# Optimization experiments

Measured on AMD Instinct MI355X. Metric: run time of the kernel, lower is better.

Reference implementation:

```python
import jax, jax.numpy as jnp
import numpy as np

N, E, D_IN, D_H, D_OUT = 100000, 1600000, 128, 128, 16


def setup_inputs() -> dict:
    key = jax.random.key(0)
    k_x, k_e, k_w1, k_w2 = jax.random.split(key, 4)
    x = jax.random.normal(k_x, (N, D_IN), dtype=jnp.float32)
    edge_index = jax.random.randint(k_e, (2, E), 0, N, dtype=jnp.int64)
    # glorot-ish init for the two GCNConv weight matrices
    W1 = jax.random.normal(k_w1, (D_IN, D_H), dtype=jnp.float32) * (1.0 / np.sqrt(D_IN))
    b1 = jnp.zeros((D_H,), dtype=jnp.float32)
    W2 = jax.random.normal(k_w2, (D_H, D_OUT), dtype=jnp.float32) * (1.0 / np.sqrt(D_H))
    b2 = jnp.zeros((D_OUT,), dtype=jnp.float32)
    return {"x": x, "edge_index": edge_index, "W1": W1, "b1": b1, "W2": W2, "b2": b2}


def _gcn_conv(x, src, dst, norm, W, b, n):
    # linear transform, gather from source nodes, normalize, scatter-add to targets
    h = x @ W                                   # [N, d_out]
    msg = h[src] * norm[:, None]                # [E+N, d_out]
    return jax.ops.segment_sum(msg, dst, num_segments=n) + b


def reference(x, edge_index, W1, b1, W2, b2):
    n = x.shape[0]
    # GCNConv default: add self-loops, symmetric normalization D^-1/2 A D^-1/2
    loops = jnp.arange(n, dtype=edge_index.dtype)
    src = jnp.concatenate([edge_index[0], loops])
    dst = jnp.concatenate([edge_index[1], loops])
    deg = jax.ops.segment_sum(jnp.ones_like(dst, dtype=x.dtype), dst, num_segments=n)
    dinv = jnp.where(deg > 0, jax.lax.rsqrt(deg), 0.0)
    norm = dinv[src] * dinv[dst]                # [E+N]

    h = _gcn_conv(x, src, dst, norm, W1, b1, n)
    h = jax.nn.relu(h)
    # dropout is identity in eval mode (reference uses eval / deterministic path)
    out = _gcn_conv(h, src, dst, norm, W2, b2, n)
    return out
```

## Files before the change

### kernel.cpp

```cpp
#include <hip/hip_runtime.h>

typedef unsigned int uint;
typedef __attribute__((ext_vector_type(8))) short bf16x8;
typedef __attribute__((ext_vector_type(4))) float f32x4;

#define D_IN 128
#define D_H  128
#define D_OUT 16
#define NPC 512
#define NPCSH 9
#define CLDS 224
#define P1 256
#define XL_STRIDE 68
#define WT_STRIDE 68

static __device__ __forceinline__ float bflo(uint u) { return __uint_as_float(u << 16); }
static __device__ __forceinline__ float bfhi(uint u) { return __uint_as_float(u & 0xFFFF0000u); }
static __device__ __forceinline__ uint f2bf(float f) {
    uint b = __float_as_uint(f);
    return (b + 0x7FFFu + ((b >> 16) & 1u)) >> 16;
}
static __device__ __forceinline__ uint pk(float a, float b) {
    return f2bf(a) | (f2bf(b) << 16);
}


__global__ __launch_bounds__(256) void k_p1hist(const int* __restrict__ dst, int E, int N, int C,
                                                int chunk, int* __restrict__ hist1,
                                                const float* __restrict__ W1,
                                                uint* __restrict__ W1p) {
    __shared__ int h[CLDS];
    int t = threadIdx.x, b = blockIdx.x;
    if (b >= P1) {
        int p = (b - P1) * 256 + t;
        int k2 = p >> 7, f = p & 127;
        float w0 = W1[(size_t)(2 * k2) * 128 + f];
        float w1 = W1[(size_t)(2 * k2 + 1) * 128 + f];
        W1p[p] = pk(w0, w1);
        return;
    }
    for (int i = t; i < C; i += 256) h[i] = 0;
    __syncthreads();
    int e0 = b * chunk, e1 = min(e0 + chunk, E);
    for (int e = e0 + t; e < e1; e += 256) {
        int d = dst[e];
        d = max(0, min(d, N - 1));
        atomicAdd(&h[d >> NPCSH], 1);
    }
    __syncthreads();
    for (int i = t; i < C; i += 256) hist1[(size_t)i * P1 + b] = h[i];
}

__global__ __launch_bounds__(1024) void k_p1scan(int* __restrict__ hist1, int C,
                                                 int* __restrict__ cbase) {
    __shared__ int col[CLDS];
    __shared__ int sdata[1024];
    int t = threadIdx.x;
    int w = t >> 6, lane = t & 63;
    for (int i = w; i < C; i += 16) {
        int4 v = ((const int4*)hist1)[i * 64 + lane];
        int s = v.x + v.y + v.z + v.w;
        int inc = s;
        for (int off = 1; off < 64; off <<= 1) {
            int o = __shfl_up(inc, off);
            if (lane >= off) inc += o;
        }
        int excl = inc - s;
        int4 p;
        p.x = excl;
        p.y = excl + v.x;
        p.z = excl + v.x + v.y;
        p.w = excl + v.x + v.y + v.z;
        ((int4*)hist1)[i * 64 + lane] = p;
        if (lane == 63) col[i] = inc;
    }
    __syncthreads();
    int v = (t < C) ? col[t] : 0;
    sdata[t] = v;
    __syncthreads();
    for (int off = 1; off < 1024; off <<= 1) {
        int x = (t >= off) ? sdata[t - off] : 0;
        __syncthreads();
        sdata[t] += x;
        __syncthreads();
    }
    int pos = sdata[t] - v;
    if (t < C) cbase[t] = pos;
    if (t == 1023) cbase[C] = sdata[1023];
    if (t < C) col[t] = pos;
    __syncthreads();
    for (int i = w; i < C; i += 16) {
        int base = col[i];
        int4 p = ((int4*)hist1)[i * 64 + lane];
        p.x += base; p.y += base; p.z += base; p.w += base;
        ((int4*)hist1)[i * 64 + lane] = p;
    }
}

__global__ __launch_bounds__(256) void k_p1fill(const int* __restrict__ src,
                                                const int* __restrict__ dst, int E, int N, int C,
                                                int chunk, const int* __restrict__ hist1,
                                                uint* __restrict__ binned1) {
    __shared__ int cur[CLDS];
    int t = threadIdx.x, b = blockIdx.x;
    for (int i = t; i < C; i += 256) cur[i] = hist1[(size_t)i * P1 + b];
    __syncthreads();
    int e0 = b * chunk, e1 = min(e0 + chunk, E);
    for (int e = e0 + t; e < e1; e += 256) {
        int d = dst[e];
        d = max(0, min(d, N - 1));
        int s = src[e];
        s = max(0, min(s, N - 1));
        int p = atomicAdd(&cur[d >> NPCSH], 1);
        binned1[p] = ((uint)(d & (NPC - 1)) << 17) | (uint)s;
    }
}


__global__ __launch_bounds__(256) void k_p2gemm1(const uint* __restrict__ binned1,
                                                 const int* __restrict__ cbase, int N, int C,
                                                 int* __restrict__ ssrc, int* __restrict__ rowptr,
                                                 int* __restrict__ deg, float* __restrict__ dinv,
                                                 const uint* __restrict__ W1p,
                                                 const float* __restrict__ x,
                                                 uint* __restrict__ hs_b, int ntiles) {
    __shared__ uint smem[128 * WT_STRIDE + 64 * XL_STRIDE];
    int t = threadIdx.x;
    if ((int)blockIdx.x < C) {
        int* ncnt = (int*)smem;
        int* nbase_ = ncnt + NPC;
        int* sdata = nbase_ + NPC;
        int c = blockIdx.x;
        int start = cbase[c], end = cbase[c + 1];
        for (int i = t; i < NPC; i += 256) ncnt[i] = 0;
        __syncthreads();
        for (int j = start + t; j < end; j += 256) atomicAdd(&ncnt[binned1[j] >> 17], 1);
        __syncthreads();
        int v0 = ncnt[2 * t], v1 = ncnt[2 * t + 1];
        int s = v0 + v1;
        sdata[t] = s;
        __syncthreads();
        for (int off = 1; off < 256; off <<= 1) {
            int xv = (t >= off) ? sdata[t - off] : 0;
            __syncthreads();
            sdata[t] += xv;
            __syncthreads();
        }
        int pre = sdata[t] - s;
        nbase_[2 * t] = start + pre;
        nbase_[2 * t + 1] = start + pre + v0;
        __syncthreads();
        for (int i = t; i < NPC; i += 256) {
            int node = c * NPC + i;
            if (node < N) {
                deg[node] = ncnt[i];
                rowptr[node] = nbase_[i];
                dinv[node] = rsqrtf((float)ncnt[i] + 1.0f);
            }
        }
        __syncthreads();
        for (int i = t; i < NPC; i += 256) ncnt[i] = nbase_[i];
        __syncthreads();
        for (int j = start + t; j < end; j += 256) {
            uint pe = binned1[j];
            int p = atomicAdd(&ncnt[pe >> 17], 1);
            ssrc[p] = (int)(pe & 0x1FFFFu);
        }
        return;
    }
    uint* Wt = smem;
    uint* xl = smem + 128 * WT_STRIDE;
    int role = blockIdx.x - C;
    int nroles = gridDim.x - C;
    for (int p = t; p < 64 * 128; p += 256) {
        int k2 = p >> 7, f = p & 127;
        Wt[f * WT_STRIDE + k2] = W1p[p];
    }
    int w = t >> 6, lane = t & 63;
    int q = lane >> 4, m = lane & 15;
    const float4* x4 = (const float4*)x;
    for (int tile = role; tile < ntiles; tile += nroles) {
        int row0 = tile * 64;
        __syncthreads();
        for (int p = t; p < 64 * 32; p += 256) {
            int r = p >> 5, c2 = p & 31;
            int gr = row0 + r;
            float4 v = (gr < N) ? x4[(size_t)gr * 32 + c2] : make_float4(0.f, 0.f, 0.f, 0.f);
            *(uint2*)&xl[r * XL_STRIDE + 2 * c2] = make_uint2(pk(v.x, v.y), pk(v.z, v.w));
        }
        __syncthreads();
        bf16x8 afr[4][4];
#pragma unroll
        for (int rt = 0; rt < 4; rt++)
#pragma unroll
            for (int kc = 0; kc < 4; kc++)
                afr[rt][kc] = *(const bf16x8*)&xl[(rt * 16 + m) * XL_STRIDE + kc * 16 + q * 4];
        f32x4 acc[2][4];
#pragma unroll
        for (int c = 0; c < 2; c++)
#pragma unroll
            for (int rt = 0; rt < 4; rt++) acc[c][rt] = (f32x4){0.f, 0.f, 0.f, 0.f};
#pragma unroll
        for (int c = 0; c < 2; c++) {
            int f = w * 32 + c * 16 + m;
#pragma unroll
            for (int kc = 0; kc < 4; kc++) {
                bf16x8 bfr = *(const bf16x8*)&Wt[f * WT_STRIDE + kc * 16 + q * 4];
#pragma unroll
                for (int rt = 0; rt < 4; rt++)
                    acc[c][rt] = __builtin_amdgcn_mfma_f32_16x16x32_bf16(afr[rt][kc], bfr,
                                                                         acc[c][rt], 0, 0, 0);
            }
        }
        __syncthreads();
        uint* outl = xl;
#pragma unroll
        for (int rt = 0; rt < 4; rt++) {
#pragma unroll
            for (int c = 0; c < 2; c++) {
                f32x4 a = acc[c][rt];
#pragma unroll
                for (int r = 0; r < 4; r++) {
                    float v = a[r];
                    float vn = __shfl_xor(v, 1);
                    if (!(lane & 1)) {
                        int row = rt * 16 + q * 4 + r;
                        int cp = (w * 32 + c * 16 + m) >> 1;
                        outl[row * 65 + cp] = pk(v, vn);
                    }
                }
            }
        }
        __syncthreads();
        for (int p = t; p < 64 * 64; p += 256) {
            int r = p >> 6, cc = p & 63;
            int gr = row0 + r;
            if (gr < N) hs_b[(size_t)gr * 64 + cc] = outl[r * 65 + cc];
        }
    }
}


__global__ __launch_bounds__(256) void k_agg1(const uint* __restrict__ hs_b,
                                              const int* __restrict__ rowptr,
                                              const int* __restrict__ deg,
                                              const int* __restrict__ ssrc,
                                              const float* __restrict__ dinv,
                                              const float2* __restrict__ b1, int N,
                                              uint* __restrict__ rh_b) {
    int w = threadIdx.x >> 6, lane = threadIdx.x & 63;
    int d = blockIdx.x * 4 + w;
    if (d >= N) return;
    int start = rowptr[d], cnt = deg[d];
    float sc = dinv[d];
    uint sv = hs_b[(size_t)d * 64 + lane];
    float a0 = bflo(sv) * sc, a1 = bfhi(sv) * sc;
    int base = 0;
    while (base < cnt) {
        int nb = min(cnt - base, 64);
        int idxv = (lane < nb) ? ssrc[start + base + lane] : 0;
        float dvv = dinv[idxv];
        int j = 0;
        for (; j + 16 <= nb; j += 16) {
            uint u[16];
            float dv[16];
#pragma unroll
            for (int q = 0; q < 16; q++) {
                int i = __shfl(idxv, j + q);
                dv[q] = __shfl(dvv, j + q);
                u[q] = hs_b[(size_t)i * 64 + lane];
            }
#pragma unroll
            for (int q = 0; q < 16; q++) {
                a0 = fmaf(bflo(u[q]), dv[q], a0);
                a1 = fmaf(bfhi(u[q]), dv[q], a1);
            }
        }
        for (; j + 4 <= nb; j += 4) {
            uint u[4];
            float dv[4];
#pragma unroll
            for (int q = 0; q < 4; q++) {
                int i = __shfl(idxv, j + q);
                dv[q] = __shfl(dvv, j + q);
                u[q] = hs_b[(size_t)i * 64 + lane];
            }
#pragma unroll
            for (int q = 0; q < 4; q++) {
                a0 = fmaf(bflo(u[q]), dv[q], a0);
                a1 = fmaf(bfhi(u[q]), dv[q], a1);
            }
        }
        for (; j < nb; j++) {
            int i = __shfl(idxv, j);
            float dv = __shfl(dvv, j);
            uint u = hs_b[(size_t)i * 64 + lane];
            a0 = fmaf(bflo(u), dv, a0);
            a1 = fmaf(bfhi(u), dv, a1);
        }
        base += nb;
    }
    float2 bb = b1[lane];
    rh_b[(size_t)d * 64 + lane] =
        pk(fmaxf(fmaf(a0, sc, bb.x), 0.f), fmaxf(fmaf(a1, sc, bb.y), 0.f));
}


__global__ __launch_bounds__(256) void k_gemm2(const uint* __restrict__ rh_b,
                                               const float* __restrict__ W2,
                                               const float* __restrict__ dinv, int N,
                                               uint* __restrict__ h2_b) {
    __shared__ float Wl[D_H * D_OUT];
    int t = threadIdx.x;
    for (int i = t; i < D_H * D_OUT; i += 256) Wl[i] = W2[i];
    __syncthreads();
    int r = blockIdx.x * 256 + t;
    if (r >= N) return;
    const uint* xrow = rh_b + (size_t)r * 64;
    float acc[16];
#pragma unroll
    for (int f = 0; f < 16; f++) acc[f] = 0.f;
    for (int c = 0; c < 16; c++) {
        uint4 xv = *(const uint4*)(xrow + c * 4);
        uint xs[4] = {xv.x, xv.y, xv.z, xv.w};
#pragma unroll
        for (int u = 0; u < 4; u++) {
            int k = c * 8 + u * 2;
            float x0 = bflo(xs[u]), x1 = bfhi(xs[u]);
            const float* w0 = &Wl[k * 16];
            const float* w1 = &Wl[(k + 1) * 16];
#pragma unroll
            for (int f = 0; f < 16; f++) acc[f] = fmaf(x0, w0[f], acc[f]);
#pragma unroll
            for (int f = 0; f < 16; f++) acc[f] = fmaf(x1, w1[f], acc[f]);
        }
    }
    float sc = dinv[r];
    uint o[8];
#pragma unroll
    for (int q = 0; q < 8; q++) o[q] = pk(acc[2 * q] * sc, acc[2 * q + 1] * sc);
    *(uint4*)&h2_b[(size_t)r * 8] = make_uint4(o[0], o[1], o[2], o[3]);
    *(uint4*)&h2_b[(size_t)r * 8 + 4] = make_uint4(o[4], o[5], o[6], o[7]);
}


__global__ __launch_bounds__(256) void k_agg2(const uint* __restrict__ h2_b,
                                              const int* __restrict__ rowptr,
                                              const int* __restrict__ deg,
                                              const int* __restrict__ ssrc,
                                              const float* __restrict__ dinv,
                                              const float* __restrict__ b2, int N,
                                              float2* __restrict__ out) {
    int w = threadIdx.x >> 6, lane = threadIdx.x & 63;
    int d = blockIdx.x * 4 + w;
    if (d >= N) return;
    int slot = lane >> 3, jp = lane & 7;
    int start = rowptr[d], cnt = deg[d];
    float a0 = 0.f, a1 = 0.f;
    if (slot == 0) {
        uint sv = h2_b[(size_t)d * 8 + jp];
        a0 = bflo(sv);
        a1 = bfhi(sv);
    }
    int base = 0;
    while (base < cnt) {
        int nb = min(cnt - base, 64);
        int idxv = (lane < nb) ? ssrc[start + base + lane] : 0;
        int ng = (nb + 7) >> 3;
        if (ng <= 4) {
            int i0 = __shfl(idxv, slot);
            int i1 = __shfl(idxv, 8 + slot);
            int i2 = __shfl(idxv, 16 + slot);
            int i3 = __shfl(idxv, 24 + slot);
            uint u0 = (slot < nb) ? h2_b[(size_t)i0 * 8 + jp] : 0u;
            uint u1 = (8 + slot < nb) ? h2_b[(size_t)i1 * 8 + jp] : 0u;
            uint u2 = (16 + slot < nb) ? h2_b[(size_t)i2 * 8 + jp] : 0u;
            uint u3 = (24 + slot < nb) ? h2_b[(size_t)i3 * 8 + jp] : 0u;
            a0 += bflo(u0) + bflo(u1) + bflo(u2) + bflo(u3);
            a1 += bfhi(u0) + bfhi(u1) + bfhi(u2) + bfhi(u3);
        } else {
            for (int g = 0; g < ng; g++) {
                int j = g * 8 + slot;
                int i = __shfl(idxv, j);
                if (j < nb) {
                    uint hv = h2_b[(size_t)i * 8 + jp];
                    a0 += bflo(hv);
                    a1 += bfhi(hv);
                }
            }
        }
        base += nb;
    }
    a0 += __shfl_xor(a0, 8);
    a1 += __shfl_xor(a1, 8);
    a0 += __shfl_xor(a0, 16);
    a1 += __shfl_xor(a1, 16);
    a0 += __shfl_xor(a0, 32);
    a1 += __shfl_xor(a1, 32);
    if (slot == 0) {
        float di = dinv[d];
        out[(size_t)d * 8 + jp] =
            make_float2(fmaf(a0, di, b2[2 * jp]), fmaf(a1, di, b2[2 * jp + 1]));
    }
}


extern "C" void kernel_launch(void* const* d_in, const int* in_sizes, int n_in,
                              void* d_out, int out_size, void* d_ws, size_t ws_size,
                              hipStream_t stream) {
    const float* x  = (const float*)d_in[0];
    const int*   ei = (const int*)d_in[1];
    const float* W1 = (const float*)d_in[2];
    const float* b1 = (const float*)d_in[3];
    const float* W2 = (const float*)d_in[4];
    const float* b2 = (const float*)d_in[5];
    int N = in_sizes[0] / D_IN;
    int E = in_sizes[1] / 2;
    const int* src = ei;
    const int* dst = ei + E;
    int C = (N + NPC - 1) / NPC;
    int chunk = (E + P1 - 1) / P1;
    int ntiles = (N + 63) / 64;

    char* ws = (char*)d_ws;
    size_t off = 0;
    auto alloc = [&](size_t bytes) -> char* {
        char* p = ws + off;
        off = (off + bytes + 255) & ~(size_t)255;
        return p;
    };
    int*   hist1   = (int*)alloc((size_t)P1 * C * 4);
    int*   cbase   = (int*)alloc((size_t)(C + 1) * 4);
    uint*  binned1 = (uint*)alloc((size_t)E * 4);
    int*   ssrc    = (int*)alloc((size_t)E * 4);
    int*   rowptr  = (int*)alloc((size_t)N * 4);
    int*   deg     = (int*)alloc((size_t)N * 4);
    float* dinv    = (float*)alloc((size_t)N * 4);
    uint*  W1p     = (uint*)alloc((size_t)64 * 128 * 4);
    uint*  hs_b    = (uint*)alloc((size_t)N * 64 * 4);
    uint*  rh_b    = (uint*)alloc((size_t)N * 64 * 4);
    uint*  h2_b    = hs_b;

    k_p1hist<<<P1 + 32, 256, 0, stream>>>(dst, E, N, C, chunk, hist1, W1, W1p);
    k_p1scan<<<1, 1024, 0, stream>>>(hist1, C, cbase);
    k_p1fill<<<P1, 256, 0, stream>>>(src, dst, E, N, C, chunk, hist1, binned1);
    int g1 = min(768, ntiles);
    k_p2gemm1<<<C + g1, 256, 0, stream>>>(binned1, cbase, N, C, ssrc, rowptr, deg, dinv,
                                          W1p, x, hs_b, ntiles);
    k_agg1<<<(N + 3) / 4, 256, 0, stream>>>(hs_b, rowptr, deg, ssrc, dinv,
                                            (const float2*)b1, N, rh_b);
    k_gemm2<<<(N + 255) / 256, 256, 0, stream>>>(rh_b, W2, dinv, N, h2_b);
    k_agg2<<<(N + 3) / 4, 256, 0, stream>>>(h2_b, rowptr, deg, ssrc, dinv, b2, N,
                                            (float2*)d_out);
}
```

Baseline: 278.5 us.

## Split layer-1 features into column halves and pin each half to an XCD group

The GEMM1 output is now stored as two column halves, each a contiguous [N,32] array of packed bf16 pairs. The aggregation kernel maps blocks so that XCDs 0-3 handle one half and XCDs 4-7 the other, and each wave processes two destination nodes with 32 lanes apiece. The aim is to halve the gathered working set per XCD so random neighbour gathers hit in each XCD's L2 more often. The cost is that a 64-lane wave now runs until the larger of its two nodes' degrees, so lanes of the smaller node sit masked, and neighbour indices are loaded twice, once per half. Correctness assumes blocks are dispatched round-robin across the 8 XCDs.

```diff
diff --git a/kernel.cpp b/kernel.cpp
--- a/kernel.cpp
+++ b/kernel.cpp
@@ -235,7 +235,9 @@
         for (int p = t; p < 64 * 64; p += 256) {
             int r = p >> 6, cc = p & 63;
             int gr = row0 + r;
-            if (gr < N) hs_b[(size_t)gr * 64 + cc] = outl[r * 65 + cc];
+            if (gr < N)
+                hs_b[(size_t)(cc >> 5) * N * 32 + (size_t)gr * 32 + (cc & 31)] =
+                    outl[r * 65 + cc];
         }
     }
 }
@@ -248,17 +250,30 @@
                                               const float* __restrict__ dinv,
                                               const float2* __restrict__ b1, int N,
                                               uint* __restrict__ rh_b) {
-    int w = threadIdx.x >> 6, lane = threadIdx.x & 63;
-    int d = blockIdx.x * 4 + w;
-    if (d >= N) return;
-    int start = rowptr[d], cnt = deg[d];
-    float sc = dinv[d];
-    uint sv = hs_b[(size_t)d * 64 + lane];
-    float a0 = bflo(sv) * sc, a1 = bfhi(sv) * sc;
+    int t = threadIdx.x;
+    int w = t >> 6, lane = t & 63;
+    int B = blockIdx.x;
+    int xcd = B & 7;
+    int half = xcd >> 2;
+    int slot = xcd & 3;
+    int g = B >> 3;
+    int d = g * 32 + slot * 8 + w * 2 + (lane >> 5);
+    bool act = (d < N);
+    int dd = act ? d : 0;
+    int start = rowptr[dd];
+    int cnt = act ? deg[dd] : 0;
+    int fl = lane & 31;
+    const uint* hsH = hs_b + (size_t)half * N * 32;
+    float scd = dinv[dd];
+    uint sv = hsH[(size_t)dd * 32 + fl];
+    float a0 = bflo(sv) * scd, a1 = bfhi(sv) * scd;
+    int cnt_o = __shfl(cnt, lane ^ 32);
+    int cmax = max(cnt, cnt_o);
     int base = 0;
-    while (base < cnt) {
-        int nb = min(cnt - base, 64);
-        int idxv = (lane < nb) ? ssrc[start + base + lane] : 0;
+    while (base < cmax) {
+        int nb = min(cmax - base, 32);
+        int nbh = min(max(cnt - base, 0), 32);
+        int idxv = (fl < nbh) ? ssrc[start + base + fl] : 0;
         float dvv = dinv[idxv];
         int j = 0;
         for (; j + 16 <= nb; j += 16) {
@@ -266,9 +281,11 @@
             float dv[16];
 #pragma unroll
             for (int q = 0; q < 16; q++) {
-                int i = __shfl(idxv, j + q);
-                dv[q] = __shfl(dvv, j + q);
-                u[q] = hs_b[(size_t)i * 64 + lane];
+                int sj = (lane & 32) | (j + q);
+                int i = __shfl(idxv, sj);
+                float dq = __shfl(dvv, sj);
+                dv[q] = (j + q < nbh) ? dq : 0.f;
+                u[q] = hsH[(size_t)i * 32 + fl];
             }
 #pragma unroll
             for (int q = 0; q < 16; q++) {
@@ -281,9 +298,11 @@
             float dv[4];
 #pragma unroll
             for (int q = 0; q < 4; q++) {
-                int i = __shfl(idxv, j + q);
-                dv[q] = __shfl(dvv, j + q);
-                u[q] = hs_b[(size_t)i * 64 + lane];
+                int sj = (lane & 32) | (j + q);
+                int i = __shfl(idxv, sj);
+                float dq = __shfl(dvv, sj);
+                dv[q] = (j + q < nbh) ? dq : 0.f;
+                u[q] = hsH[(size_t)i * 32 + fl];
             }
 #pragma unroll
             for (int q = 0; q < 4; q++) {
@@ -292,17 +311,21 @@
             }
         }
         for (; j < nb; j++) {
-            int i = __shfl(idxv, j);
-            float dv = __shfl(dvv, j);
-            uint u = hs_b[(size_t)i * 64 + lane];
+            int sj = (lane & 32) | j;
+            int i = __shfl(idxv, sj);
+            float dq = __shfl(dvv, sj);
+            float dv = (j < nbh) ? dq : 0.f;
+            uint u = hsH[(size_t)i * 32 + fl];
             a0 = fmaf(bflo(u), dv, a0);
             a1 = fmaf(bfhi(u), dv, a1);
         }
         base += nb;
     }
-    float2 bb = b1[lane];
-    rh_b[(size_t)d * 64 + lane] =
-        pk(fmaxf(fmaf(a0, sc, bb.x), 0.f), fmaxf(fmaf(a1, sc, bb.y), 0.f));
+    if (act) {
+        float2 bb = b1[half * 32 + fl];
+        rh_b[(size_t)dd * 64 + half * 32 + fl] =
+            pk(fmaxf(fmaf(a0, scd, bb.x), 0.f), fmaxf(fmaf(a1, scd, bb.y), 0.f));
+    }
 }
 
 
@@ -447,8 +470,9 @@
     int g1 = min(768, ntiles);
     k_p2gemm1<<<C + g1, 256, 0, stream>>>(binned1, cbase, N, C, ssrc, rowptr, deg, dinv,
                                           W1p, x, hs_b, ntiles);
-    k_agg1<<<(N + 3) / 4, 256, 0, stream>>>(hs_b, rowptr, deg, ssrc, dinv,
-                                            (const float2*)b1, N, rh_b);
+    int groups = (N + 31) / 32;
+    k_agg1<<<groups * 8, 256, 0, stream>>>(hs_b, rowptr, deg, ssrc, dinv,
+                                           (const float2*)b1, N, rh_b);
     k_gemm2<<<(N + 255) / 256, 256, 0, stream>>>(rh_b, W2, dinv, N, h2_b);
     k_agg2<<<(N + 3) / 4, 256, 0, stream>>>(h2_b, rowptr, deg, ssrc, dinv, b2, N,
                                             (float2*)d_out);
```

Result: faster. 272.0 us, median of 2 (-2.3%).
